# Kernel optimization log

Hardware: AMD Instinct MI355X
Metric: run time of the kernel (lower is better)

The kernel has to match this reference:

```python
import jax, jax.numpy as jnp
import numpy as np

N_PTS = 8_388_608
WIDTH, HEIGHT = 1232.0, 1616.0
K3 = jnp.array([[758.03967, 0.0, 621.46572],
                [0.0, 761.62359, 756.86402],
                [0.0, 0.0, 1.0]], dtype=jnp.float32)
MIN_D_R, MAX_D_R = 1.0, 10.0   # rewards_from_pose defaults
MIN_D_M, MAX_D_M = 1.0, 5.0    # Model pc_clip_limits
DELTA = 0.05
EPS = 1e-6


def euler_xyz(roll, pitch, yaw):
    # pytorch3d euler_angles_to_matrix(angles, 'XYZ') = Rx(roll) @ Ry(pitch) @ Rz(yaw)
    cr, sr = jnp.cos(roll), jnp.sin(roll)
    cp, sp = jnp.cos(pitch), jnp.sin(pitch)
    cy, sy = jnp.cos(yaw), jnp.sin(yaw)
    one, zero = jnp.ones_like(cr), jnp.zeros_like(cr)
    Rx = jnp.array([[one, zero, zero], [zero, cr, -sr], [zero, sr, cr]])
    Ry = jnp.array([[cp, zero, sp], [zero, one, zero], [-sp, zero, cp]])
    Rz = jnp.array([[cy, -sy, zero], [sy, cy, zero], [zero, zero, one]])
    return Rx @ Ry @ Rz


def reward_from_pose(pose, verts):
    # pose: [6] = (x, y, z, roll, pitch, yaw); verts: [N,3]
    x, y, z, roll, pitch, yaw = pose[0], pose[1], pose[2], pose[3], pose[4], pose[5]
    R = euler_xyz(roll, pitch, yaw)                 # [3,3]
    t = jnp.stack([x, y, z])                        # [3]
    v = (verts - t) @ R                             # R_inv @ p == p @ R (R orthonormal); [N,3]
    dist_mask = (v[:, 2] > MIN_D_R) & (v[:, 2] < MAX_D_R)
    p = v @ K3.T                                    # homogeneous image coords [N,3]
    u = p[:, 0] / p[:, 2]
    w = p[:, 1] / p[:, 2]
    fov_mask = (p[:, 2] > 0) & (u > 1) & (u < WIDTH - 1) & (w > 1) & (w < HEIGHT - 1)
    return jnp.sum(dist_mask & fov_mask).astype(jnp.float32)


def setup_inputs() -> dict:
    key = jax.random.key(0)
    points = 5.0 * jax.random.normal(key, (N_PTS, 3), dtype=jnp.float32)
    z0 = jnp.float32(0.0)
    return {"points": points, "x": z0, "y": z0, "z": z0,
            "roll": z0, "pitch": z0, "yaw": z0}


def reference(points, x, y, z, roll, pitch, yaw):
    pose0 = jnp.stack([x, y, z, roll, pitch, yaw])
    # 7 poses: baseline + 6 finite-difference perturbations (as in FrustumVisibilityEst.forward)
    poses = jnp.concatenate([pose0[None], pose0[None] + DELTA * jnp.eye(6, dtype=pose0.dtype)], axis=0)
    rewards = jax.vmap(reward_from_pose, in_axes=(0, None))(poses, points)  # [7]
    reward = rewards[0]
    loss = 1.0 / (reward + EPS)

    # Model.forward geometry path (uses pc_clip_limits = [1, 5])
    R = euler_xyz(roll, pitch, yaw)
    t = jnp.stack([x, y, z])
    vc = (points - t) @ R                           # camera-frame verts [N,3]
    dist_mask = (vc[:, 2] > MIN_D_M) & (vc[:, 2] < MAX_D_M)
    p = vc @ K3.T
    u = p[:, 0] / p[:, 2]
    w = p[:, 1] / p[:, 2]
    fov_mask = (p[:, 2] > 0) & (u > 1) & (u < WIDTH - 1) & (w > 1) & (w < HEIGHT - 1)
    mask = dist_mask & fov_mask
    # original does verts[mask]; we zero out masked-off rows to keep static shapes
    verts_out = jnp.where(mask[:, None], vc, jnp.zeros((), vc.dtype))
    return verts_out, loss
```

## Files before the change

kernel.cpp:

```cpp
#include <hip/hip_runtime.h>

#define N_PTS 8388608
#define FX 758.03967f
#define CXC 621.46572f
#define FY 761.62359f
#define CYC 756.86402f
#define U_MAX 1231.0f
#define W_MAX 1615.0f
#define MIN_D 1.0f
#define MAX_D_R 10.0f
#define MAX_D_M 5.0f

#define N_SLOTS 64
#define SLOT_STRIDE 32

typedef float nfloat4 __attribute__((ext_vector_type(4)));


__global__ void pose_setup_kernel(const float* __restrict__ x, const float* __restrict__ y,
                                  const float* __restrict__ z, const float* __restrict__ roll,
                                  const float* __restrict__ pitch, const float* __restrict__ yaw,
                                  float* __restrict__ ws) {
    int tid = threadIdx.x;
    if (tid == 0) {
        float cr = cosf(*roll), sr = sinf(*roll);
        float cp = cosf(*pitch), sp = sinf(*pitch);
        float cy = cosf(*yaw),  sy = sinf(*yaw);
        ws[0] = cp * cy;                ws[1] = -(cp * sy);             ws[2] = sp;
        ws[3] = cr * sy + sr * sp * cy; ws[4] = cr * cy - sr * sp * sy; ws[5] = -(sr * cp);
        ws[6] = sr * sy - cr * sp * cy; ws[7] = sr * cy + cr * sp * sy; ws[8] = cr * cp;
        ws[9] = *x; ws[10] = *y; ws[11] = *z;
    }
    if (tid < N_SLOTS) {
        ((unsigned int*)ws)[16 + tid * SLOT_STRIDE] = 0u;
    }
}

__global__ __launch_bounds__(256) void frustum_kernel(const float4* __restrict__ pts,
                                                      const float* __restrict__ ws,
                                                      float4* __restrict__ out) {
    const float R0 = ws[0], R1 = ws[1], R2 = ws[2];
    const float R3 = ws[3], R4 = ws[4], R5 = ws[5];
    const float R6 = ws[6], R7 = ws[7], R8 = ws[8];
    const float t0 = ws[9], t1 = ws[10], t2 = ws[11];

    const int tid = blockIdx.x * 256 + threadIdx.x;
    const long base = (long)tid * 3;
    float4 q0 = pts[base + 0];
    float4 q1 = pts[base + 1];
    float4 q2 = pts[base + 2];

    int cnt = 0;
    auto proc = [&](float px, float py, float pz, float& ox, float& oy, float& oz) {
        float d0 = px - t0, d1 = py - t1, d2 = pz - t2;
        float v0 = fmaf(d2, R6, fmaf(d1, R3, d0 * R0));
        float v1 = fmaf(d2, R7, fmaf(d1, R4, d0 * R1));
        float v2 = fmaf(d2, R8, fmaf(d1, R5, d0 * R2));
        float p0 = fmaf(v2, CXC, v0 * FX);
        float p1 = fmaf(v2, CYC, v1 * FY);
        float u = p0 / v2;
        float w = p1 / v2;
        bool fov = (v2 > 0.0f) && (u > 1.0f) && (u < U_MAX) && (w > 1.0f) && (w < W_MAX);
        if (fov && (v2 > MIN_D) && (v2 < MAX_D_R)) cnt++;
        bool m = fov && (v2 > MIN_D) && (v2 < MAX_D_M);
        ox = m ? v0 : 0.0f;
        oy = m ? v1 : 0.0f;
        oz = m ? v2 : 0.0f;
    };

    float4 o0, o1, o2;
    proc(q0.x, q0.y, q0.z, o0.x, o0.y, o0.z);
    proc(q0.w, q1.x, q1.y, o0.w, o1.x, o1.y);
    proc(q1.z, q1.w, q2.x, o1.z, o1.w, o2.x);
    proc(q2.y, q2.z, q2.w, o2.y, o2.z, o2.w);

    __builtin_nontemporal_store(*(const nfloat4*)&o0, (nfloat4*)&out[base + 0]);
    __builtin_nontemporal_store(*(const nfloat4*)&o1, (nfloat4*)&out[base + 1]);
    __builtin_nontemporal_store(*(const nfloat4*)&o2, (nfloat4*)&out[base + 2]);

    for (int off = 32; off > 0; off >>= 1) cnt += __shfl_down(cnt, off, 64);
    __shared__ int red[4];
    const int wave = threadIdx.x >> 6;
    if ((threadIdx.x & 63) == 0) red[wave] = cnt;
    __syncthreads();
    if (threadIdx.x == 0) {
        int s = red[0] + red[1] + red[2] + red[3];
        if (s > 0) {
            unsigned int* slot = (unsigned int*)ws + 16 + (blockIdx.x & (N_SLOTS - 1)) * SLOT_STRIDE;
            atomicAdd(slot, (unsigned int)s);
        }
    }
}

__global__ void finalize_kernel(const float* __restrict__ ws, float* __restrict__ out) {
    unsigned int c = 0;
    for (int i = 0; i < N_SLOTS; ++i)
        c += ((const unsigned int*)ws)[16 + i * SLOT_STRIDE];
    out[(long)3 * N_PTS] = 1.0f / ((float)c + 1e-6f);
}

extern "C" void kernel_launch(void* const* d_in, const int* in_sizes, int n_in,
                              void* d_out, int out_size, void* d_ws, size_t ws_size,
                              hipStream_t stream) {
    const float* points = (const float*)d_in[0];
    const float* x      = (const float*)d_in[1];
    const float* y      = (const float*)d_in[2];
    const float* z      = (const float*)d_in[3];
    const float* roll   = (const float*)d_in[4];
    const float* pitch  = (const float*)d_in[5];
    const float* yaw    = (const float*)d_in[6];
    float* ws = (float*)d_ws;
    float* out = (float*)d_out;

    pose_setup_kernel<<<1, 64, 0, stream>>>(x, y, z, roll, pitch, yaw, ws);

    const int threads = 256;
    const int n_thread_units = N_PTS / 4;
    const int blocks = n_thread_units / threads;
    frustum_kernel<<<blocks, threads, 0, stream>>>((const float4*)points, ws, (float4*)out);

    finalize_kernel<<<1, 1, 0, stream>>>(ws, out);
}
```

Measured before the change: 233.1 us.

## Fuse pose setup and finalize into main kernel via last-block ticket

Each block now computes the rotation matrix and translation itself into shared memory. The separate finalize kernel is replaced by a last-block-done pattern that uses an atomic ticket counter and thread fences. Together these remove two dependent launches, keeping only a small init kernel that zeroes the counters. Nontemporal stores are also replaced with ordinary stores, which could change cache behaviour on the write stream. The cost is redundant trig work and an extra atomic in every block.

```diff
diff --git a/kernel.cpp b/kernel.cpp
--- a/kernel.cpp
+++ b/kernel.cpp
@@ -13,42 +13,47 @@
 
 #define N_SLOTS 64
 #define SLOT_STRIDE 32
-
-typedef float nfloat4 __attribute__((ext_vector_type(4)));
+#define N_BLOCKS (N_PTS / 4 / 256)
 
 
-__global__ void pose_setup_kernel(const float* __restrict__ x, const float* __restrict__ y,
-                                  const float* __restrict__ z, const float* __restrict__ roll,
-                                  const float* __restrict__ pitch, const float* __restrict__ yaw,
-                                  float* __restrict__ ws) {
+__global__ void init_kernel(float* __restrict__ ws) {
     int tid = threadIdx.x;
-    if (tid == 0) {
-        float cr = cosf(*roll), sr = sinf(*roll);
-        float cp = cosf(*pitch), sp = sinf(*pitch);
-        float cy = cosf(*yaw),  sy = sinf(*yaw);
-        ws[0] = cp * cy;                ws[1] = -(cp * sy);             ws[2] = sp;
-        ws[3] = cr * sy + sr * sp * cy; ws[4] = cr * cy - sr * sp * sy; ws[5] = -(sr * cp);
-        ws[6] = sr * sy - cr * sp * cy; ws[7] = sr * cy + cr * sp * sy; ws[8] = cr * cp;
-        ws[9] = *x; ws[10] = *y; ws[11] = *z;
-    }
-    if (tid < N_SLOTS) {
-        ((unsigned int*)ws)[16 + tid * SLOT_STRIDE] = 0u;
-    }
+    if (tid < N_SLOTS) ((unsigned int*)ws)[16 + tid * SLOT_STRIDE] = 0u;
+    if (tid == 0)      ((unsigned int*)ws)[14] = 0u;
 }
 
 __global__ __launch_bounds__(256) void frustum_kernel(const float4* __restrict__ pts,
-                                                      const float* __restrict__ ws,
+                                                      const float* __restrict__ x,
+                                                      const float* __restrict__ y,
+                                                      const float* __restrict__ z,
+                                                      const float* __restrict__ roll,
+                                                      const float* __restrict__ pitch,
+                                                      const float* __restrict__ yaw,
+                                                      float* __restrict__ ws,
                                                       float4* __restrict__ out) {
-    const float R0 = ws[0], R1 = ws[1], R2 = ws[2];
-    const float R3 = ws[3], R4 = ws[4], R5 = ws[5];
-    const float R6 = ws[6], R7 = ws[7], R8 = ws[8];
-    const float t0 = ws[9], t1 = ws[10], t2 = ws[11];
+    __shared__ float S[12];
 
     const int tid = blockIdx.x * 256 + threadIdx.x;
     const long base = (long)tid * 3;
     float4 q0 = pts[base + 0];
     float4 q1 = pts[base + 1];
     float4 q2 = pts[base + 2];
+
+    if (threadIdx.x == 0) {
+        float cr = cosf(*roll), sr = sinf(*roll);
+        float cp = cosf(*pitch), sp = sinf(*pitch);
+        float cy = cosf(*yaw),  sy = sinf(*yaw);
+        S[0] = cp * cy;                S[1] = -(cp * sy);             S[2] = sp;
+        S[3] = cr * sy + sr * sp * cy; S[4] = cr * cy - sr * sp * sy; S[5] = -(sr * cp);
+        S[6] = sr * sy - cr * sp * cy; S[7] = sr * cy + cr * sp * sy; S[8] = cr * cp;
+        S[9] = *x; S[10] = *y; S[11] = *z;
+    }
+    __syncthreads();
+
+    const float R0 = S[0], R1 = S[1], R2 = S[2];
+    const float R3 = S[3], R4 = S[4], R5 = S[5];
+    const float R6 = S[6], R7 = S[7], R8 = S[8];
+    const float t0 = S[9], t1 = S[10], t2 = S[11];
 
     int cnt = 0;
     auto proc = [&](float px, float py, float pz, float& ox, float& oy, float& oz) {
@@ -74,9 +79,9 @@
     proc(q1.z, q1.w, q2.x, o1.z, o1.w, o2.x);
     proc(q2.y, q2.z, q2.w, o2.y, o2.z, o2.w);
 
-    __builtin_nontemporal_store(*(const nfloat4*)&o0, (nfloat4*)&out[base + 0]);
-    __builtin_nontemporal_store(*(const nfloat4*)&o1, (nfloat4*)&out[base + 1]);
-    __builtin_nontemporal_store(*(const nfloat4*)&o2, (nfloat4*)&out[base + 2]);
+    out[base + 0] = o0;
+    out[base + 1] = o1;
+    out[base + 2] = o2;
 
     for (int off = 32; off > 0; off >>= 1) cnt += __shfl_down(cnt, off, 64);
     __shared__ int red[4];
@@ -85,18 +90,21 @@
     __syncthreads();
     if (threadIdx.x == 0) {
         int s = red[0] + red[1] + red[2] + red[3];
+        unsigned int* slots = (unsigned int*)ws + 16;
         if (s > 0) {
-            unsigned int* slot = (unsigned int*)ws + 16 + (blockIdx.x & (N_SLOTS - 1)) * SLOT_STRIDE;
-            atomicAdd(slot, (unsigned int)s);
+            atomicAdd(slots + (blockIdx.x & (N_SLOTS - 1)) * SLOT_STRIDE, (unsigned int)s);
+        }
+        __threadfence();
+        unsigned int ticket = atomicAdd((unsigned int*)ws + 14, 1u);
+        if (ticket == (unsigned int)(gridDim.x - 1)) {
+            __threadfence();
+            unsigned int c = 0;
+            for (int i = 0; i < N_SLOTS; ++i)
+                c += __hip_atomic_load(slots + i * SLOT_STRIDE,
+                                       __ATOMIC_RELAXED, __HIP_MEMORY_SCOPE_AGENT);
+            ((float*)out)[(long)3 * N_PTS] = 1.0f / ((float)c + 1e-6f);
         }
     }
-}
-
-__global__ void finalize_kernel(const float* __restrict__ ws, float* __restrict__ out) {
-    unsigned int c = 0;
-    for (int i = 0; i < N_SLOTS; ++i)
-        c += ((const unsigned int*)ws)[16 + i * SLOT_STRIDE];
-    out[(long)3 * N_PTS] = 1.0f / ((float)c + 1e-6f);
 }
 
 extern "C" void kernel_launch(void* const* d_in, const int* in_sizes, int n_in,
@@ -112,12 +120,10 @@
     float* ws = (float*)d_ws;
     float* out = (float*)d_out;
 
-    pose_setup_kernel<<<1, 64, 0, stream>>>(x, y, z, roll, pitch, yaw, ws);
+    init_kernel<<<1, 64, 0, stream>>>(ws);
 
     const int threads = 256;
-    const int n_thread_units = N_PTS / 4;
-    const int blocks = n_thread_units / threads;
-    frustum_kernel<<<blocks, threads, 0, stream>>>((const float4*)points, ws, (float4*)out);
-
-    finalize_kernel<<<1, 1, 0, stream>>>(ws, out);
+    frustum_kernel<<<N_BLOCKS, threads, 0, stream>>>((const float4*)points,
+                                                     x, y, z, roll, pitch, yaw,
+                                                     ws, (float4*)out);
 }
```

New measurement: 695.4 us. 2.98x slower.
